# Kernel optimization log

Measured on AMD Instinct MI355X. Metric: run time of the kernel, lower is better.

## Reference

```python
import jax, jax.numpy as jnp
import numpy as np
from jax import lax

B, T, I, H, L = 2048, 2048, 1, 16, 2  # batch, seq, input_dim, hidden_dim, n_layers


def setup_inputs() -> dict:
    key = jax.random.key(0)
    ks = jax.random.split(key, 9)
    s = 1.0 / np.sqrt(H)  # PyTorch nn.LSTM init range
    u = lambda k, shape: jax.random.uniform(k, shape, jnp.float32, -s, s)
    return {
        "x": jax.random.normal(ks[0], (B, T, I), jnp.float32),
        "h0": jnp.zeros((L, B, H), jnp.float32),
        "c0": jnp.zeros((L, B, H), jnp.float32),
        "W_ih0": u(ks[1], (4 * H, I)),
        "W_hh0": u(ks[2], (4 * H, H)),
        "b_ih0": u(ks[3], (4 * H,)),
        "b_hh0": u(ks[4], (4 * H,)),
        "W_ih1": u(ks[5], (4 * H, H)),
        "W_hh1": u(ks[6], (4 * H, H)),
        "b_ih1": u(ks[7], (4 * H,)),
        "b_hh1": u(ks[8], (4 * H,)),
    }


def _lstm_layer(x, h0, c0, Wih, Whh, bih, bhh):
    # Precompute input contribution for all timesteps: [B,T,4H]
    pre = jnp.einsum('bti,gi->btg', x, Wih) + bih + bhh

    def step(carry, xt):
        h, c = carry
        g = xt + h @ Whh.T                       # [B,4H]
        i, f, gg, o = jnp.split(g, 4, axis=-1)   # PyTorch gate order i,f,g,o
        i = jax.nn.sigmoid(i)
        f = jax.nn.sigmoid(f)
        gg = jnp.tanh(gg)
        o = jax.nn.sigmoid(o)
        c = f * c + i * gg
        h = o * jnp.tanh(c)
        return (h, c), h

    (hT, cT), hs = lax.scan(step, (h0, c0), pre.transpose(1, 0, 2))
    return hs.transpose(1, 0, 2), hT, cT  # [B,T,H], [B,H], [B,H]


def reference(x, h0, c0, W_ih0, W_hh0, b_ih0, b_hh0, W_ih1, W_hh1, b_ih1, b_hh1):
    out0, h1, c1 = _lstm_layer(x, h0[0], c0[0], W_ih0, W_hh0, b_ih0, b_hh0)
    out1, h2, c2 = _lstm_layer(out0, h0[1], c0[1], W_ih1, W_hh1, b_ih1, b_hh1)
    hN = jnp.stack([h1, h2])  # [L,B,H]
    cN = jnp.stack([c1, c2])  # [L,B,H]
    return out1, (hN, cN)
```

## Files before the change

### kernel.cpp

```cpp
#include <hip/hip_runtime.h>

#define BB 2048
#define TT 2048
#define HH 16

__device__ __forceinline__ float rl(float v, int l) {
    return __int_as_float(__builtin_amdgcn_readlane(__float_as_int(v), l));
}
__device__ __forceinline__ float bperm(int byteaddr, float v) {
    return __int_as_float(__builtin_amdgcn_ds_bpermute(byteaddr, __float_as_int(v)));
}
__device__ __forceinline__ float fexp2(float x) {
#if __has_builtin(__builtin_amdgcn_exp2f)
    return __builtin_amdgcn_exp2f(x);
#else
    return exp2f(x);
#endif
}
__device__ __forceinline__ float frcp(float x) {
#if __has_builtin(__builtin_amdgcn_rcpf)
    return __builtin_amdgcn_rcpf(x);
#else
    return 1.0f / x;
#endif
}

#define L2E  1.442695041f
#define L2E2 2.885390082f

__global__ __launch_bounds__(256, 2) void lstm2_kernel(
    const float* __restrict__ x,
    const float* __restrict__ h0in,
    const float* __restrict__ c0in,
    const float* __restrict__ Wih0,
    const float* __restrict__ Whh0,
    const float* __restrict__ bih0,
    const float* __restrict__ bhh0,
    const float* __restrict__ Wih1,
    const float* __restrict__ Whh1,
    const float* __restrict__ bih1,
    const float* __restrict__ bhh1,
    float* __restrict__ out)
{
    const int lane = threadIdx.x & 63;
    const int wid  = threadIdx.x >> 6;
    const int b    = blockIdx.x * 4 + wid;
    const int j    = lane & 15;

    float w0[16], wi1[16], w1[16];
#pragma unroll
    for (int k = 0; k < 16; ++k) {
        w0[k]  = Whh0[lane * 16 + k];
        wi1[k] = Wih1[lane * 16 + k];
        w1[k]  = Whh1[lane * 16 + k];
    }
    const float wx    = Wih0[lane];
    const float bias0 = bih0[lane] + bhh0[lane];
    const float bias1 = bih1[lane] + bhh1[lane];

    float h0 = h0in[0 * BB * HH + b * HH + j];
    float c0 = c0in[0 * BB * HH + b * HH + j];
    float h1 = h0in[1 * BB * HH + b * HH + j];
    float c1 = c0in[1 * BB * HH + b * HH + j];

    float sh0[16], sh1[16];
#pragma unroll
    for (int k = 0; k < 16; ++k) { sh0[k] = rl(h0, k); sh1[k] = rl(h1, k); }

    const bool is_tanh = ((lane >> 4) == 2);
    const float Aa = is_tanh ? 2.0f  : 1.0f;
    const float Bb = is_tanh ? -L2E2 : -L2E;
    const float Cc = is_tanh ? -1.0f : 0.0f;

    const int ai = j * 4, af = ai + 64, ag = ai + 128, ao = ai + 192;

    const int  phase   = lane >> 4;
    float hist = 0.0f;

    const float* xp = x + (size_t)b * TT;
    float*       po = out + (size_t)b * TT * HH;

    for (int t0 = 0; t0 < TT; t0 += 64) {
        int xraw = __float_as_int(xp[t0 + lane]);

#pragma unroll 4
        for (int tt = 0; tt < 64; ++tt) {
            float xt = __int_as_float(__builtin_amdgcn_readlane(xraw, tt));

            float A0 = fmaf(xt, wx, bias0), A1 = 0.0f;
#pragma unroll
            for (int k = 0; k < 16; k += 2) {
                A0 = fmaf(sh0[k],     w0[k],     A0);
                A1 = fmaf(sh0[k + 1], w0[k + 1], A1);
            }
            float acc = A0 + A1;
            float act = fmaf(Aa, frcp(1.0f + fexp2(Bb * acc)), Cc);

            float i_ = bperm(ai, act);
            float f_ = bperm(af, act);
            float g_ = bperm(ag, act);
            float o_ = bperm(ao, act);
            c0 = fmaf(f_, c0, i_ * g_);
            float tc0 = fmaf(2.0f, frcp(1.0f + fexp2(-L2E2 * c0)), -1.0f);
            h0 = o_ * tc0;

#pragma unroll
            for (int k = 0; k < 16; ++k) sh0[k] = rl(h0, k);

            float B0 = bias1, B1 = 0.0f;
#pragma unroll
            for (int k = 0; k < 16; k += 2) {
                B0 = fmaf(sh0[k],     wi1[k],     B0);
                B1 = fmaf(sh0[k + 1], wi1[k + 1], B1);
            }
#pragma unroll
            for (int k = 0; k < 16; k += 2) {
                B0 = fmaf(sh1[k],     w1[k],     B0);
                B1 = fmaf(sh1[k + 1], w1[k + 1], B1);
            }
            float acc1 = B0 + B1;
            float act1 = fmaf(Aa, frcp(1.0f + fexp2(Bb * acc1)), Cc);

            float i1 = bperm(ai, act1);
            float f1 = bperm(af, act1);
            float g1 = bperm(ag, act1);
            float o1 = bperm(ao, act1);
            c1 = fmaf(f1, c1, i1 * g1);
            float tc1 = fmaf(2.0f, frcp(1.0f + fexp2(-L2E2 * c1)), -1.0f);
            h1 = o1 * tc1;

#pragma unroll
            for (int k = 0; k < 16; ++k) sh1[k] = rl(h1, k);

            hist = (phase == (tt & 3)) ? h1 : hist;
            if ((tt & 3) == 3) {
                po[(size_t)(t0 + tt - 3) * HH + lane] = hist;
            }
        }
    }

    if (lane < 16) {
        const size_t offH = (size_t)BB * TT * HH;
        const size_t offC = offH + (size_t)2 * BB * HH;
        out[offH + 0 * BB * HH + b * HH + lane] = h0;
        out[offH + 1 * BB * HH + b * HH + lane] = h1;
        out[offC + 0 * BB * HH + b * HH + lane] = c0;
        out[offC + 1 * BB * HH + b * HH + lane] = c1;
    }
}

extern "C" void kernel_launch(void* const* d_in, const int* in_sizes, int n_in,
                              void* d_out, int out_size, void* d_ws, size_t ws_size,
                              hipStream_t stream) {
    const float* x    = (const float*)d_in[0];
    const float* h0   = (const float*)d_in[1];
    const float* c0   = (const float*)d_in[2];
    const float* Wih0 = (const float*)d_in[3];
    const float* Whh0 = (const float*)d_in[4];
    const float* bih0 = (const float*)d_in[5];
    const float* bhh0 = (const float*)d_in[6];
    const float* Wih1 = (const float*)d_in[7];
    const float* Whh1 = (const float*)d_in[8];
    const float* bih1 = (const float*)d_in[9];
    const float* bhh1 = (const float*)d_in[10];
    float* out = (float*)d_out;

    dim3 grid(BB / 4);
    dim3 block(256);
    lstm2_kernel<<<grid, block, 0, stream>>>(x, h0, c0, Wih0, Whh0, bih0, bhh0,
                                             Wih1, Whh1, bih1, bhh1, out);
}
```

Measured before the change: 1.178 ms.

## Skew LSTM layers across timesteps, broadcast h via LDS, use packed FMA

Layer 1 now runs one timestep behind layer 0, with a prologue and epilogue to cover the edges. Both layers' matvecs, activations and cell updates become independent within one iteration and can interleave, which shortens the serial dependency chain per step. The hidden-state broadcast moves from 16 readlanes per layer to an LDS store followed by vector LDS reads. The dot products use v_pk_fma_f32 on paired weights. The LDS round trip relies on wave-synchronous ordering without an explicit barrier, and the inline asm limits what the compiler can schedule.

```diff
diff --git a/kernel.cpp b/kernel.cpp
--- a/kernel.cpp
+++ b/kernel.cpp
@@ -4,9 +4,9 @@
 #define TT 2048
 #define HH 16
 
-__device__ __forceinline__ float rl(float v, int l) {
-    return __int_as_float(__builtin_amdgcn_readlane(__float_as_int(v), l));
-}
+typedef __attribute__((ext_vector_type(2))) float f32x2;
+typedef __attribute__((ext_vector_type(4))) float f32x4;
+
 __device__ __forceinline__ float bperm(int byteaddr, float v) {
     return __int_as_float(__builtin_amdgcn_ds_bpermute(byteaddr, __float_as_int(v)));
 }
@@ -24,6 +24,11 @@
     return 1.0f / x;
 #endif
 }
+__device__ __forceinline__ void pkfma(f32x2& a, f32x2 b, f32x2 c) {
+    asm("v_pk_fma_f32 %0, %1, %2, %0" : "+v"(a) : "v"(b), "v"(c));
+}
+__device__ __forceinline__ f32x2 lo2(f32x4 v) { return __builtin_shufflevector(v, v, 0, 1); }
+__device__ __forceinline__ f32x2 hi2(f32x4 v) { return __builtin_shufflevector(v, v, 2, 3); }
 
 #define L2E  1.442695041f
 #define L2E2 2.885390082f
@@ -47,103 +52,147 @@
     const int b    = blockIdx.x * 4 + wid;
     const int j    = lane & 15;
 
-    float w0[16], wi1[16], w1[16];
-#pragma unroll
-    for (int k = 0; k < 16; ++k) {
-        w0[k]  = Whh0[lane * 16 + k];
-        wi1[k] = Wih1[lane * 16 + k];
-        w1[k]  = Whh1[lane * 16 + k];
+    __shared__ __align__(16) float lds[4][2][64];
+    float* l0 = lds[wid][0];
+    float* l1 = lds[wid][1];
+    const f32x4* r0 = (const f32x4*)(l0 + (lane & 48));
+    const f32x4* r1 = (const f32x4*)(l1 + (lane & 48));
+
+    f32x2 w0p[8], wi1p[8], w1p[8];
+    {
+        const f32x4* p0 = (const f32x4*)Whh0 + lane * 4;
+        const f32x4* p1 = (const f32x4*)Wih1 + lane * 4;
+        const f32x4* p2 = (const f32x4*)Whh1 + lane * 4;
+#pragma unroll
+        for (int r = 0; r < 4; ++r) {
+            f32x4 a = p0[r], c = p1[r], d = p2[r];
+            w0p[2*r] = lo2(a);  w0p[2*r+1] = hi2(a);
+            wi1p[2*r] = lo2(c); wi1p[2*r+1] = hi2(c);
+            w1p[2*r] = lo2(d);  w1p[2*r+1] = hi2(d);
+        }
     }
     const float wx    = Wih0[lane];
     const float bias0 = bih0[lane] + bhh0[lane];
     const float bias1 = bih1[lane] + bhh1[lane];
 
-    float h0 = h0in[0 * BB * HH + b * HH + j];
-    float c0 = c0in[0 * BB * HH + b * HH + j];
-    float h1 = h0in[1 * BB * HH + b * HH + j];
-    float c1 = c0in[1 * BB * HH + b * HH + j];
-
-    float sh0[16], sh1[16];
-#pragma unroll
-    for (int k = 0; k < 16; ++k) { sh0[k] = rl(h0, k); sh1[k] = rl(h1, k); }
+    float h0v = h0in[0 * BB * HH + b * HH + j];
+    float c0  = c0in[0 * BB * HH + b * HH + j];
+    float h1v = h0in[1 * BB * HH + b * HH + j];
+    float c1  = c0in[1 * BB * HH + b * HH + j];
+
+    l0[lane] = h0v;
+    l1[lane] = h1v;
+    __builtin_amdgcn_sched_barrier(0);
+    f32x4 hb0[4], hb1[4];
+#pragma unroll
+    for (int r = 0; r < 4; ++r) { hb0[r] = r0[r]; hb1[r] = r1[r]; }
 
     const bool is_tanh = ((lane >> 4) == 2);
     const float Aa = is_tanh ? 2.0f  : 1.0f;
     const float Bb = is_tanh ? -L2E2 : -L2E;
     const float Cc = is_tanh ? -1.0f : 0.0f;
-
     const int ai = j * 4, af = ai + 64, ag = ai + 128, ao = ai + 192;
-
-    const int  phase   = lane >> 4;
+    const int phase = lane >> 4;
     float hist = 0.0f;
 
     const float* xp = x + (size_t)b * TT;
     float*       po = out + (size_t)b * TT * HH;
 
-    for (int t0 = 0; t0 < TT; t0 += 64) {
-        int xraw = __float_as_int(xp[t0 + lane]);
+    {
+        float xt = xp[0];
+        f32x2 a = { fmaf(xt, wx, bias0), 0.0f };
+#pragma unroll
+        for (int r = 0; r < 4; ++r) {
+            pkfma(a, w0p[2*r],   lo2(hb0[r]));
+            pkfma(a, w0p[2*r+1], hi2(hb0[r]));
+        }
+        float acc = a.x + a.y;
+        float act = fmaf(Aa, frcp(1.0f + fexp2(Bb * acc)), Cc);
+        float i_ = bperm(ai, act), f_ = bperm(af, act), g_ = bperm(ag, act), o_ = bperm(ao, act);
+        c0  = fmaf(f_, c0, i_ * g_);
+        h0v = o_ * fmaf(2.0f, frcp(1.0f + fexp2(-L2E2 * c0)), -1.0f);
+        l0[lane] = h0v;
+        __builtin_amdgcn_sched_barrier(0);
+#pragma unroll
+        for (int r = 0; r < 4; ++r) hb0[r] = r0[r];
+    }
+
+    int xnext = __float_as_int(xp[1 + lane]);
+    int xcur  = 0;
 
 #pragma unroll 4
-        for (int tt = 0; tt < 64; ++tt) {
-            float xt = __int_as_float(__builtin_amdgcn_readlane(xraw, tt));
-
-            float A0 = fmaf(xt, wx, bias0), A1 = 0.0f;
-#pragma unroll
-            for (int k = 0; k < 16; k += 2) {
-                A0 = fmaf(sh0[k],     w0[k],     A0);
-                A1 = fmaf(sh0[k + 1], w0[k + 1], A1);
-            }
-            float acc = A0 + A1;
-            float act = fmaf(Aa, frcp(1.0f + fexp2(Bb * acc)), Cc);
-
-            float i_ = bperm(ai, act);
-            float f_ = bperm(af, act);
-            float g_ = bperm(ag, act);
-            float o_ = bperm(ao, act);
-            c0 = fmaf(f_, c0, i_ * g_);
-            float tc0 = fmaf(2.0f, frcp(1.0f + fexp2(-L2E2 * c0)), -1.0f);
-            h0 = o_ * tc0;
-
-#pragma unroll
-            for (int k = 0; k < 16; ++k) sh0[k] = rl(h0, k);
-
-            float B0 = bias1, B1 = 0.0f;
-#pragma unroll
-            for (int k = 0; k < 16; k += 2) {
-                B0 = fmaf(sh0[k],     wi1[k],     B0);
-                B1 = fmaf(sh0[k + 1], wi1[k + 1], B1);
-            }
-#pragma unroll
-            for (int k = 0; k < 16; k += 2) {
-                B0 = fmaf(sh1[k],     w1[k],     B0);
-                B1 = fmaf(sh1[k + 1], w1[k + 1], B1);
-            }
-            float acc1 = B0 + B1;
-            float act1 = fmaf(Aa, frcp(1.0f + fexp2(Bb * acc1)), Cc);
-
-            float i1 = bperm(ai, act1);
-            float f1 = bperm(af, act1);
-            float g1 = bperm(ag, act1);
-            float o1 = bperm(ao, act1);
-            c1 = fmaf(f1, c1, i1 * g1);
-            float tc1 = fmaf(2.0f, frcp(1.0f + fexp2(-L2E2 * c1)), -1.0f);
-            h1 = o1 * tc1;
-
-#pragma unroll
-            for (int k = 0; k < 16; ++k) sh1[k] = rl(h1, k);
-
-            hist = (phase == (tt & 3)) ? h1 : hist;
-            if ((tt & 3) == 3) {
-                po[(size_t)(t0 + tt - 3) * HH + lane] = hist;
-            }
-        }
+    for (int k = 0; k < TT - 1; ++k) {
+        if ((k & 63) == 0) {
+            xcur = xnext;
+            int idx = k + 65 + lane; if (idx > TT - 1) idx = TT - 1;
+            xnext = __float_as_int(xp[idx]);
+        }
+        float xt = __int_as_float(__builtin_amdgcn_readlane(xcur, k & 63));
+
+        f32x2 a  = { fmaf(xt, wx, bias0), 0.0f };
+        f32x2 bb = { bias1, 0.0f };
+#pragma unroll
+        for (int r = 0; r < 4; ++r) {
+            f32x2 hlo = lo2(hb0[r]), hhi = hi2(hb0[r]);
+            pkfma(a,  w0p[2*r],    hlo);
+            pkfma(a,  w0p[2*r+1],  hhi);
+            pkfma(bb, wi1p[2*r],   hlo);
+            pkfma(bb, wi1p[2*r+1], hhi);
+        }
+#pragma unroll
+        for (int r = 0; r < 4; ++r) {
+            pkfma(bb, w1p[2*r],   lo2(hb1[r]));
+            pkfma(bb, w1p[2*r+1], hi2(hb1[r]));
+        }
+        float acc0 = a.x + a.y;
+        float acc1 = bb.x + bb.y;
+        float act0 = fmaf(Aa, frcp(1.0f + fexp2(Bb * acc0)), Cc);
+        float act1 = fmaf(Aa, frcp(1.0f + fexp2(Bb * acc1)), Cc);
+
+        float i0 = bperm(ai, act0), f0 = bperm(af, act0), g0 = bperm(ag, act0), o0 = bperm(ao, act0);
+        float i1 = bperm(ai, act1), f1 = bperm(af, act1), g1 = bperm(ag, act1), o1 = bperm(ao, act1);
+
+        c0  = fmaf(f0, c0, i0 * g0);
+        h0v = o0 * fmaf(2.0f, frcp(1.0f + fexp2(-L2E2 * c0)), -1.0f);
+        c1  = fmaf(f1, c1, i1 * g1);
+        h1v = o1 * fmaf(2.0f, frcp(1.0f + fexp2(-L2E2 * c1)), -1.0f);
+
+        l0[lane] = h0v;
+        l1[lane] = h1v;
+        __builtin_amdgcn_sched_barrier(0);
+#pragma unroll
+        for (int r = 0; r < 4; ++r) { hb0[r] = r0[r]; hb1[r] = r1[r]; }
+
+        hist = (phase == (k & 3)) ? h1v : hist;
+        if ((k & 3) == 3) po[(size_t)(k - 3) * HH + lane] = hist;
+    }
+
+    {
+        f32x2 bb = { bias1, 0.0f };
+#pragma unroll
+        for (int r = 0; r < 4; ++r) {
+            pkfma(bb, wi1p[2*r],   lo2(hb0[r]));
+            pkfma(bb, wi1p[2*r+1], hi2(hb0[r]));
+        }
+#pragma unroll
+        for (int r = 0; r < 4; ++r) {
+            pkfma(bb, w1p[2*r],   lo2(hb1[r]));
+            pkfma(bb, w1p[2*r+1], hi2(hb1[r]));
+        }
+        float acc1 = bb.x + bb.y;
+        float act1 = fmaf(Aa, frcp(1.0f + fexp2(Bb * acc1)), Cc);
+        float i1 = bperm(ai, act1), f1 = bperm(af, act1), g1 = bperm(ag, act1), o1 = bperm(ao, act1);
+        c1  = fmaf(f1, c1, i1 * g1);
+        h1v = o1 * fmaf(2.0f, frcp(1.0f + fexp2(-L2E2 * c1)), -1.0f);
+        hist = (phase == 3) ? h1v : hist;
+        po[(size_t)(TT - 4) * HH + lane] = hist;
     }
 
     if (lane < 16) {
         const size_t offH = (size_t)BB * TT * HH;
         const size_t offC = offH + (size_t)2 * BB * HH;
-        out[offH + 0 * BB * HH + b * HH + lane] = h0;
-        out[offH + 1 * BB * HH + b * HH + lane] = h1;
+        out[offH + 0 * BB * HH + b * HH + lane] = h0v;
+        out[offH + 1 * BB * HH + b * HH + lane] = h1v;
         out[offC + 0 * BB * HH + b * HH + lane] = c0;
         out[offC + 1 * BB * HH + b * HH + lane] = c1;
     }
```

Result: faster. 1.013 ms (-14.0%).

## Skew LSTM layers by one timestep and use permlane swaps for gate gather

Applied to the files above, without the earlier changes.

Restructures the recurrence so layer 0 at step t+1 and layer 1 at step t run in the same iteration, with a prologue and epilogue, doubling independent work per step to hide latency in the serial chain. It replaces the four ds_bpermute gate gathers with permlane32/permlane16 swap builtins when available, prefetches x one chunk ahead, and pins weights in VGPRs with empty asm. In exchange, register pressure rises and the final-state stores change from lane<16 guarded writes to all lanes writing redundant values.

```diff
diff --git a/kernel.cpp b/kernel.cpp
--- a/kernel.cpp
+++ b/kernel.cpp
@@ -27,6 +27,25 @@
 
 #define L2E  1.442695041f
 #define L2E2 2.885390082f
+
+#if __has_builtin(__builtin_amdgcn_permlane32_swap) && __has_builtin(__builtin_amdgcn_permlane16_swap)
+#define USE_PERMLANE 1
+#endif
+
+__device__ __forceinline__ void gates4(float act, int ai,
+                                       float& i_, float& f_, float& g_, float& o_) {
+#ifdef USE_PERMLANE
+    unsigned a = __float_as_uint(act);
+    auto pq  = __builtin_amdgcn_permlane32_swap(a, a, false, false);
+    auto if2 = __builtin_amdgcn_permlane16_swap(pq[0], pq[0], false, false);
+    auto go2 = __builtin_amdgcn_permlane16_swap(pq[1], pq[1], false, false);
+    i_ = __uint_as_float(if2[0]); f_ = __uint_as_float(if2[1]);
+    g_ = __uint_as_float(go2[0]); o_ = __uint_as_float(go2[1]);
+#else
+    i_ = bperm(ai, act); f_ = bperm(ai + 64, act);
+    g_ = bperm(ai + 128, act); o_ = bperm(ai + 192, act);
+#endif
+}
 
 __global__ __launch_bounds__(256, 2) void lstm2_kernel(
     const float* __restrict__ x,
@@ -54,98 +73,130 @@
         wi1[k] = Wih1[lane * 16 + k];
         w1[k]  = Whh1[lane * 16 + k];
     }
-    const float wx    = Wih0[lane];
-    const float bias0 = bih0[lane] + bhh0[lane];
-    const float bias1 = bih1[lane] + bhh1[lane];
-
-    float h0 = h0in[0 * BB * HH + b * HH + j];
-    float c0 = c0in[0 * BB * HH + b * HH + j];
-    float h1 = h0in[1 * BB * HH + b * HH + j];
-    float c1 = c0in[1 * BB * HH + b * HH + j];
+    float wx    = Wih0[lane];
+    float bias0 = bih0[lane] + bhh0[lane];
+    float bias1 = bih1[lane] + bhh1[lane];
+
+#pragma unroll
+    for (int k = 0; k < 16; ++k) {
+        asm("" : "+v"(w0[k]), "+v"(wi1[k]), "+v"(w1[k]));
+    }
+    asm("" : "+v"(wx), "+v"(bias0), "+v"(bias1));
+
+    float h0v = h0in[0 * BB * HH + b * HH + j];
+    float c0  = c0in[0 * BB * HH + b * HH + j];
+    float h1v = h0in[1 * BB * HH + b * HH + j];
+    float c1  = c0in[1 * BB * HH + b * HH + j];
 
     float sh0[16], sh1[16];
 #pragma unroll
-    for (int k = 0; k < 16; ++k) { sh0[k] = rl(h0, k); sh1[k] = rl(h1, k); }
+    for (int k = 0; k < 16; ++k) { sh0[k] = rl(h0v, k); sh1[k] = rl(h1v, k); }
 
     const bool is_tanh = ((lane >> 4) == 2);
     const float Aa = is_tanh ? 2.0f  : 1.0f;
     const float Bb = is_tanh ? -L2E2 : -L2E;
     const float Cc = is_tanh ? -1.0f : 0.0f;
-
-    const int ai = j * 4, af = ai + 64, ag = ai + 128, ao = ai + 192;
-
-    const int  phase   = lane >> 4;
+    const int ai = j * 4;
+    const int phase = lane >> 4;
     float hist = 0.0f;
 
     const float* xp = x + (size_t)b * TT;
     float*       po = out + (size_t)b * TT * HH;
 
-    for (int t0 = 0; t0 < TT; t0 += 64) {
-        int xraw = __float_as_int(xp[t0 + lane]);
+    {
+        float xt = xp[0];
+        float A0 = fmaf(xt, wx, bias0), A1 = 0.0f;
+#pragma unroll
+        for (int k = 0; k < 16; k += 2) {
+            A0 = fmaf(sh0[k],     w0[k],     A0);
+            A1 = fmaf(sh0[k + 1], w0[k + 1], A1);
+        }
+        float acc = A0 + A1;
+        float act = fmaf(Aa, frcp(1.0f + fexp2(Bb * acc)), Cc);
+        float i_, f_, g_, o_;
+        gates4(act, ai, i_, f_, g_, o_);
+        c0  = fmaf(f_, c0, i_ * g_);
+        h0v = o_ * fmaf(2.0f, frcp(1.0f + fexp2(-L2E2 * c0)), -1.0f);
+#pragma unroll
+        for (int k = 0; k < 16; ++k) sh0[k] = rl(h0v, k);
+    }
+
+    int xnext = __float_as_int(xp[1 + lane]);
+    int xcur  = 0;
 
 #pragma unroll 4
-        for (int tt = 0; tt < 64; ++tt) {
-            float xt = __int_as_float(__builtin_amdgcn_readlane(xraw, tt));
-
-            float A0 = fmaf(xt, wx, bias0), A1 = 0.0f;
-#pragma unroll
-            for (int k = 0; k < 16; k += 2) {
-                A0 = fmaf(sh0[k],     w0[k],     A0);
-                A1 = fmaf(sh0[k + 1], w0[k + 1], A1);
-            }
-            float acc = A0 + A1;
-            float act = fmaf(Aa, frcp(1.0f + fexp2(Bb * acc)), Cc);
-
-            float i_ = bperm(ai, act);
-            float f_ = bperm(af, act);
-            float g_ = bperm(ag, act);
-            float o_ = bperm(ao, act);
-            c0 = fmaf(f_, c0, i_ * g_);
-            float tc0 = fmaf(2.0f, frcp(1.0f + fexp2(-L2E2 * c0)), -1.0f);
-            h0 = o_ * tc0;
-
-#pragma unroll
-            for (int k = 0; k < 16; ++k) sh0[k] = rl(h0, k);
-
-            float B0 = bias1, B1 = 0.0f;
-#pragma unroll
-            for (int k = 0; k < 16; k += 2) {
-                B0 = fmaf(sh0[k],     wi1[k],     B0);
-                B1 = fmaf(sh0[k + 1], wi1[k + 1], B1);
-            }
-#pragma unroll
-            for (int k = 0; k < 16; k += 2) {
-                B0 = fmaf(sh1[k],     w1[k],     B0);
-                B1 = fmaf(sh1[k + 1], w1[k + 1], B1);
-            }
-            float acc1 = B0 + B1;
-            float act1 = fmaf(Aa, frcp(1.0f + fexp2(Bb * acc1)), Cc);
-
-            float i1 = bperm(ai, act1);
-            float f1 = bperm(af, act1);
-            float g1 = bperm(ag, act1);
-            float o1 = bperm(ao, act1);
-            c1 = fmaf(f1, c1, i1 * g1);
-            float tc1 = fmaf(2.0f, frcp(1.0f + fexp2(-L2E2 * c1)), -1.0f);
-            h1 = o1 * tc1;
-
-#pragma unroll
-            for (int k = 0; k < 16; ++k) sh1[k] = rl(h1, k);
-
-            hist = (phase == (tt & 3)) ? h1 : hist;
-            if ((tt & 3) == 3) {
-                po[(size_t)(t0 + tt - 3) * HH + lane] = hist;
-            }
-        }
-    }
-
-    if (lane < 16) {
+    for (int k = 0; k < TT - 1; ++k) {
+        if ((k & 63) == 0) {
+            xcur = xnext;
+            int idx = k + 65 + lane; if (idx > TT - 1) idx = TT - 1;
+            xnext = __float_as_int(xp[idx]);
+        }
+        float xt = __int_as_float(__builtin_amdgcn_readlane(xcur, k & 63));
+
+        float A0 = fmaf(xt, wx, bias0), A1 = 0.0f;
+        float B0 = bias1, B1 = 0.0f;
+#pragma unroll
+        for (int kk = 0; kk < 16; kk += 2) {
+            A0 = fmaf(sh0[kk],     w0[kk],      A0);
+            A1 = fmaf(sh0[kk + 1], w0[kk + 1],  A1);
+            B0 = fmaf(sh0[kk],     wi1[kk],     B0);
+            B1 = fmaf(sh0[kk + 1], wi1[kk + 1], B1);
+        }
+#pragma unroll
+        for (int kk = 0; kk < 16; kk += 2) {
+            B0 = fmaf(sh1[kk],     w1[kk],     B0);
+            B1 = fmaf(sh1[kk + 1], w1[kk + 1], B1);
+        }
+        float acc0 = A0 + A1;
+        float acc1 = B0 + B1;
+        float act0 = fmaf(Aa, frcp(1.0f + fexp2(Bb * acc0)), Cc);
+        float act1 = fmaf(Aa, frcp(1.0f + fexp2(Bb * acc1)), Cc);
+
+        float i0, f0, g0, o0, i1, f1, g1, o1;
+        gates4(act0, ai, i0, f0, g0, o0);
+        gates4(act1, ai, i1, f1, g1, o1);
+
+        c0  = fmaf(f0, c0, i0 * g0);
+        h0v = o0 * fmaf(2.0f, frcp(1.0f + fexp2(-L2E2 * c0)), -1.0f);
+        c1  = fmaf(f1, c1, i1 * g1);
+        h1v = o1 * fmaf(2.0f, frcp(1.0f + fexp2(-L2E2 * c1)), -1.0f);
+
+#pragma unroll
+        for (int kk = 0; kk < 16; ++kk) { sh0[kk] = rl(h0v, kk); sh1[kk] = rl(h1v, kk); }
+
+        hist = (phase == (k & 3)) ? h1v : hist;
+        if ((k & 3) == 3) po[(size_t)(k - 3) * HH + lane] = hist;
+    }
+
+    {
+        float B0 = bias1, B1 = 0.0f;
+#pragma unroll
+        for (int kk = 0; kk < 16; kk += 2) {
+            B0 = fmaf(sh0[kk],     wi1[kk],     B0);
+            B1 = fmaf(sh0[kk + 1], wi1[kk + 1], B1);
+        }
+#pragma unroll
+        for (int kk = 0; kk < 16; kk += 2) {
+            B0 = fmaf(sh1[kk],     w1[kk],     B0);
+            B1 = fmaf(sh1[kk + 1], w1[kk + 1], B1);
+        }
+        float acc1 = B0 + B1;
+        float act1 = fmaf(Aa, frcp(1.0f + fexp2(Bb * acc1)), Cc);
+        float i1, f1, g1, o1;
+        gates4(act1, ai, i1, f1, g1, o1);
+        c1  = fmaf(f1, c1, i1 * g1);
+        h1v = o1 * fmaf(2.0f, frcp(1.0f + fexp2(-L2E2 * c1)), -1.0f);
+        hist = (phase == 3) ? h1v : hist;
+        po[(size_t)(TT - 4) * HH + lane] = hist;
+    }
+
+    {
         const size_t offH = (size_t)BB * TT * HH;
         const size_t offC = offH + (size_t)2 * BB * HH;
-        out[offH + 0 * BB * HH + b * HH + lane] = h0;
-        out[offH + 1 * BB * HH + b * HH + lane] = h1;
-        out[offC + 0 * BB * HH + b * HH + lane] = c0;
-        out[offC + 1 * BB * HH + b * HH + lane] = c1;
+        out[offH + 0 * BB * HH + b * HH + j] = h0v;
+        out[offH + 1 * BB * HH + b * HH + j] = h1v;
+        out[offC + 0 * BB * HH + b * HH + j] = c0;
+        out[offC + 1 * BB * HH + b * HH + j] = c1;
     }
 }
 
```

After: 1.321 ms. 1.12x slower.
